# Optimization experiments

Hardware: AMD Instinct MI355X
Metric: run time of the kernel (lower is better)

Reference implementation:

```python
import jax, jax.numpy as jnp
import numpy as np

B, C_IN, C_OUT, HID, HW = 128, 1024, 1024, 256, 32

def setup_inputs() -> dict:
    key = jax.random.key(0)
    ks = jax.random.split(key, 5)
    inp = {
        "input": jax.random.normal(ks[0], (B, C_IN, HW, HW), dtype=jnp.float32),
        "fc1_w": jax.random.normal(ks[1], (HID, C_IN), dtype=jnp.float32) * 0.02,
        "fc1_b": jnp.ones((HID,), dtype=jnp.float32),
        "fc2_w": jax.random.normal(ks[2], (C_OUT, HID), dtype=jnp.float32) * (np.sqrt(2.0 / HID)),
        "fc2_b": jnp.ones((C_OUT,), dtype=jnp.float32),
        "noise": jax.random.normal(ks[3], (B, C_OUT), dtype=jnp.float32),
        "swap_idx": jax.random.randint(ks[4], (C_OUT // 2,), 0, B, dtype=jnp.int64 if jax.config.read('jax_enable_x64') else jnp.int32),
    }
    return inp

def reference(input, fc1_w, fc1_b, fc2_w, fc2_b, noise, swap_idx):
    # global average pool over H, W -> [B, C_in]
    x = jnp.mean(input, axis=(2, 3))
    y = jax.nn.relu(x @ fc1_w.T + fc1_b)          # [B, HID]
    y2 = y @ fc2_w.T + fc2_b                      # [B, C_out]
    g = noise + y2
    v1 = jnp.clip(1.2 * jax.nn.sigmoid(g) - 0.1, 0.0, 1.0)
    v2 = (g > 0).astype(v1.dtype)
    # semhash: overwrite random batch rows of v1 with hard-binarized v2
    swapped = v1.at[swap_idx].set(v2[swap_idx])
    # straight-through: forward uses swapped values, backward is identity w.r.t. v1
    out = v1 + jax.lax.stop_gradient(swapped - v1)
    return out[:, :, None, None]                  # [B, C_out, 1, 1]
```

## Files before the change

### kernel.cpp

```cpp
#include <hip/hip_runtime.h>
#include <cstdint>

#define NB    128
#define NCIN  1024
#define NCOUT 1024
#define NHID  256
#define NHW   1024

#define WARM_BLOCKS 16
#define GAP_BLOCKS  ((NB * NCIN) / 16)

typedef float f32x4 __attribute__((ext_vector_type(4)));

__global__ __launch_bounds__(256) void gap_kernel(const float* __restrict__ in,
                                                  float* __restrict__ x,
                                                  const float* __restrict__ w1,
                                                  const float* __restrict__ w2,
                                                  const float* __restrict__ noise) {
    if (blockIdx.x < WARM_BLOCKS) {
        const int start = blockIdx.x * 256 + threadIdx.x;
        float acc = 0.f;
        const float4* p1 = reinterpret_cast<const float4*>(w1);
        const float4* p2 = reinterpret_cast<const float4*>(w2);
        const float4* pn = reinterpret_cast<const float4*>(noise);
        for (int i = start; i < (NHID * NCIN) / 4; i += WARM_BLOCKS * 256) {
            float4 v = p1[i]; acc += (v.x + v.y) + (v.z + v.w);
        }
        for (int i = start; i < (NCOUT * NHID) / 4; i += WARM_BLOCKS * 256) {
            float4 v = p2[i]; acc += (v.x + v.y) + (v.z + v.w);
        }
        for (int i = start; i < (NB * NCOUT) / 4; i += WARM_BLOCKS * 256) {
            float4 v = pn[i]; acc += (v.x + v.y) + (v.z + v.w);
        }
        asm volatile("" :: "v"(acc));
        return;
    }

    const int wave = ((blockIdx.x - WARM_BLOCKS) * 256 + threadIdx.x) >> 6;
    const int lane = threadIdx.x & 63;
    const int row0 = wave * 4;
    const f32x4* base = reinterpret_cast<const f32x4*>(in);
#pragma unroll
    for (int r = 0; r < 4; ++r) {
        const f32x4* p = base + (size_t)(row0 + r) * (NHW / 4);
        f32x4 v0 = __builtin_nontemporal_load(p + lane);
        f32x4 v1 = __builtin_nontemporal_load(p + lane + 64);
        f32x4 v2 = __builtin_nontemporal_load(p + lane + 128);
        f32x4 v3 = __builtin_nontemporal_load(p + lane + 192);
        float t0 = (v0.x + v0.y) + (v0.z + v0.w);
        float t1 = (v1.x + v1.y) + (v1.z + v1.w);
        float t2 = (v2.x + v2.y) + (v2.z + v2.w);
        float t3 = (v3.x + v3.y) + (v3.z + v3.w);
        double s = ((double)t0 + (double)t1) + ((double)t2 + (double)t3);
#pragma unroll
        for (int off = 32; off > 0; off >>= 1)
            s += __shfl_down(s, off, 64);
        if (lane == 0) x[row0 + r] = (float)(s * (1.0 / 1024.0));
    }
}

__global__ __launch_bounds__(256) void fc1_kernel(const float* __restrict__ x,
                                                  const float* __restrict__ w1,
                                                  const float* __restrict__ b1,
                                                  float* __restrict__ y) {
    __shared__ float4 xs4[8][33];
    const int b  = blockIdx.x >> 3;
    const int ho = blockIdx.x & 7;
    const int t  = threadIdx.x;

    {
        float4 v = reinterpret_cast<const float4*>(x + (size_t)b * NCIN)[t];
        xs4[t >> 5][t & 31] = v;
    }
    __syncthreads();

    const int hl = t >> 3;
    const int cs = t & 7;
    const int h  = ho * 32 + hl;
    const float4* w = reinterpret_cast<const float4*>(w1 + (size_t)h * NCIN + cs * 128);
    double a0 = 0.0, a1 = 0.0, a2 = 0.0, a3 = 0.0;
#pragma unroll
    for (int i = 0; i < 32; ++i) {
        float4 wv = w[i];
        float4 xv = xs4[cs][i];
        a0 += (double)wv.x * (double)xv.x;
        a1 += (double)wv.y * (double)xv.y;
        a2 += (double)wv.z * (double)xv.z;
        a3 += (double)wv.w * (double)xv.w;
    }
    double s = (a0 + a1) + (a2 + a3);
    s += __shfl_xor(s, 1, 64);
    s += __shfl_xor(s, 2, 64);
    s += __shfl_xor(s, 4, 64);
    if (cs == 0) {
        double v = s + (double)b1[h];
        y[(size_t)b * NHID + h] = (float)(v > 0.0 ? v : 0.0);
    }
}

__global__ __launch_bounds__(256) void fc2_kernel(const float* __restrict__ y,
                                                  const float* __restrict__ w2,
                                                  const float* __restrict__ b2,
                                                  const float* __restrict__ noise,
                                                  const int* __restrict__ swap_idx,
                                                  int n_swap,
                                                  float* __restrict__ out) {
    __shared__ float ys[NHID];
    __shared__ int flag;
    const int b  = blockIdx.x >> 3;
    const int jo = blockIdx.x & 7;
    const int t  = threadIdx.x;

    if (t == 0) flag = 0;
    ys[t] = y[(size_t)b * NHID + t];
    __syncthreads();
    for (int i = t; i < n_swap; i += 256)
        if (swap_idx[i] == b) flag = 1;
    __syncthreads();
    const bool sw = (flag != 0);

    const int jl = t >> 1;
    const int ch = t & 1;
    const int j  = jo * 128 + jl;
    const float4* w  = reinterpret_cast<const float4*>(w2 + (size_t)j * NHID + ch * 128);
    const float*  yp = ys + ch * 128;
    double a0 = 0.0, a1 = 0.0, a2 = 0.0, a3 = 0.0;
#pragma unroll
    for (int i = 0; i < 32; ++i) {
        float4 wv = w[i];
        a0 += (double)wv.x * (double)yp[4 * i + 0];
        a1 += (double)wv.y * (double)yp[4 * i + 1];
        a2 += (double)wv.z * (double)yp[4 * i + 2];
        a3 += (double)wv.w * (double)yp[4 * i + 3];
    }
    double s = (a0 + a1) + (a2 + a3);
    s += __shfl_xor(s, 1, 64);
    if (ch == 0) {
        double g = s + (double)b2[j] + (double)noise[(size_t)b * NCOUT + j];
        float gf  = (float)g;
        float sig = 1.0f / (1.0f + __expf(-gf));
        float v1  = fminf(fmaxf(1.2f * sig - 0.1f, 0.0f), 1.0f);
        float v2  = (g > 0.0) ? 1.0f : 0.0f;
        out[(size_t)b * NCOUT + j] = sw ? v2 : v1;
    }
}

extern "C" void kernel_launch(void* const* d_in, const int* in_sizes, int n_in,
                              void* d_out, int out_size, void* d_ws, size_t ws_size,
                              hipStream_t stream) {
    const float* input = (const float*)d_in[0];
    const float* fc1_w = (const float*)d_in[1];
    const float* fc1_b = (const float*)d_in[2];
    const float* fc2_w = (const float*)d_in[3];
    const float* fc2_b = (const float*)d_in[4];
    const float* noise = (const float*)d_in[5];
    const int*   swap  = (const int*)d_in[6];
    const int n_swap = in_sizes[6];

    float* x = (float*)d_ws;
    float* y = x + NB * NCIN;

    gap_kernel<<<WARM_BLOCKS + GAP_BLOCKS, 256, 0, stream>>>(input, x, fc1_w,
                                                             fc2_w, noise);
    fc1_kernel<<<NB * 8, 256, 0, stream>>>(x, fc1_w, fc1_b, y);
    fc2_kernel<<<NB * 8, 256, 0, stream>>>(y, fc2_w, fc2_b, noise, swap, n_swap,
                                           (float*)d_out);
}
```

Measured before the change: 119.0 us.

## Drop warm-up blocks, use plain loads and LDS-based row reduction in GAP

Removes the extra warm-up blocks that prefetched the FC weights and noise into cache during the pooling kernel. Replaces nontemporal loads with ordinary loads. Moves the per-row final reduction from a 6-step double shuffle chain per row into a shared-memory stage followed by a 4-step shuffle across 16 lanes. This aims to cut shuffle latency and the extra block work, but the later FC kernels lose their warm cache, and the added LDS and barrier cost something.

Result: slower. 134.9 us (+13.4%).

```diff
diff --git a/kernel.cpp b/kernel.cpp
--- a/kernel.cpp
+++ b/kernel.cpp
@@ -7,56 +7,40 @@
 #define NHID  256
 #define NHW   1024
 
-#define WARM_BLOCKS 16
-#define GAP_BLOCKS  ((NB * NCIN) / 16)
-
 typedef float f32x4 __attribute__((ext_vector_type(4)));
 
 __global__ __launch_bounds__(256) void gap_kernel(const float* __restrict__ in,
-                                                  float* __restrict__ x,
-                                                  const float* __restrict__ w1,
-                                                  const float* __restrict__ w2,
-                                                  const float* __restrict__ noise) {
-    if (blockIdx.x < WARM_BLOCKS) {
-        const int start = blockIdx.x * 256 + threadIdx.x;
-        float acc = 0.f;
-        const float4* p1 = reinterpret_cast<const float4*>(w1);
-        const float4* p2 = reinterpret_cast<const float4*>(w2);
-        const float4* pn = reinterpret_cast<const float4*>(noise);
-        for (int i = start; i < (NHID * NCIN) / 4; i += WARM_BLOCKS * 256) {
-            float4 v = p1[i]; acc += (v.x + v.y) + (v.z + v.w);
-        }
-        for (int i = start; i < (NCOUT * NHID) / 4; i += WARM_BLOCKS * 256) {
-            float4 v = p2[i]; acc += (v.x + v.y) + (v.z + v.w);
-        }
-        for (int i = start; i < (NB * NCOUT) / 4; i += WARM_BLOCKS * 256) {
-            float4 v = pn[i]; acc += (v.x + v.y) + (v.z + v.w);
-        }
-        asm volatile("" :: "v"(acc));
-        return;
-    }
+                                                  float* __restrict__ x) {
+    __shared__ float part[16][65];
+    const int w    = threadIdx.x >> 6;
+    const int lane = threadIdx.x & 63;
+    const int rowBase = blockIdx.x * 16;
+    const f32x4* base = reinterpret_cast<const f32x4*>(in);
 
-    const int wave = ((blockIdx.x - WARM_BLOCKS) * 256 + threadIdx.x) >> 6;
-    const int lane = threadIdx.x & 63;
-    const int row0 = wave * 4;
-    const f32x4* base = reinterpret_cast<const f32x4*>(in);
 #pragma unroll
     for (int r = 0; r < 4; ++r) {
-        const f32x4* p = base + (size_t)(row0 + r) * (NHW / 4);
-        f32x4 v0 = __builtin_nontemporal_load(p + lane);
-        f32x4 v1 = __builtin_nontemporal_load(p + lane + 64);
-        f32x4 v2 = __builtin_nontemporal_load(p + lane + 128);
-        f32x4 v3 = __builtin_nontemporal_load(p + lane + 192);
+        const f32x4* p = base + (size_t)(rowBase + w * 4 + r) * (NHW / 4);
+        f32x4 v0 = p[lane];
+        f32x4 v1 = p[lane + 64];
+        f32x4 v2 = p[lane + 128];
+        f32x4 v3 = p[lane + 192];
         float t0 = (v0.x + v0.y) + (v0.z + v0.w);
         float t1 = (v1.x + v1.y) + (v1.z + v1.w);
         float t2 = (v2.x + v2.y) + (v2.z + v2.w);
         float t3 = (v3.x + v3.y) + (v3.z + v3.w);
-        double s = ((double)t0 + (double)t1) + ((double)t2 + (double)t3);
-#pragma unroll
-        for (int off = 32; off > 0; off >>= 1)
-            s += __shfl_down(s, off, 64);
-        if (lane == 0) x[row0 + r] = (float)(s * (1.0 / 1024.0));
+        part[w * 4 + r][lane] = (t0 + t1) + (t2 + t3);
     }
+    __syncthreads();
+
+    const int row = threadIdx.x >> 4;
+    const int seg = threadIdx.x & 15;
+    double s = ((double)part[row][seg * 4 + 0] + (double)part[row][seg * 4 + 1])
+             + ((double)part[row][seg * 4 + 2] + (double)part[row][seg * 4 + 3]);
+    s += __shfl_xor(s, 1, 64);
+    s += __shfl_xor(s, 2, 64);
+    s += __shfl_xor(s, 4, 64);
+    s += __shfl_xor(s, 8, 64);
+    if (seg == 0) x[rowBase + row] = (float)(s * (1.0 / 1024.0));
 }
 
 __global__ __launch_bounds__(256) void fc1_kernel(const float* __restrict__ x,
@@ -160,8 +144,7 @@
     float* x = (float*)d_ws;
     float* y = x + NB * NCIN;
 
-    gap_kernel<<<WARM_BLOCKS + GAP_BLOCKS, 256, 0, stream>>>(input, x, fc1_w,
-                                                             fc2_w, noise);
+    gap_kernel<<<(NB * NCIN) / 16, 256, 0, stream>>>(input, x);
     fc1_kernel<<<NB * 8, 256, 0, stream>>>(x, fc1_w, fc1_b, y);
     fc2_kernel<<<NB * 8, 256, 0, stream>>>(y, fc2_w, fc2_b, noise, swap, n_swap,
                                            (float*)d_out);
```
